# Kernel tuning notes

Hardware: AMD Instinct MI355X
Metric: run time of the kernel (lower is better)

## Reference

```python
import jax, jax.numpy as jnp
import numpy as np

# Model config (mirrors init_kwargs)
E = 8          # num_experts
K = 2          # top_k
S = 1          # select_top_k
THRESHOLD = 0.7
NORM_TOPK = True
H = 1024       # hidden_dim
F = 1024       # moe intermediate dim
B, SEQ = 2, 1024


def setup_inputs() -> dict:
    key = jax.random.key(0)
    k1, k2, k3, k4, k5 = jax.random.split(key, 5)
    hidden_states = jax.random.normal(k1, (B, SEQ, H), jnp.float32)
    gate_weight = jax.random.normal(k2, (E, H), jnp.float32) * 0.02
    gate_up_proj = jax.random.normal(k3, (E, 2 * F, H), jnp.float32) * 0.02
    down_proj = jax.random.normal(k4, (E, H, F), jnp.float32) * 0.02
    sim = jax.random.uniform(k5, (E, E), jnp.float32)
    sim = (sim + sim.T) / 2.0
    sim = sim.at[jnp.arange(E), jnp.arange(E)].set(1.0)  # fill_diagonal_(1.0)
    return {
        "hidden_states": hidden_states,
        "gate_weight": gate_weight,
        "gate_up_proj": gate_up_proj,
        "down_proj": down_proj,
        "similarity_matrix": sim,
    }


def reference(hidden_states, gate_weight, gate_up_proj, down_proj, similarity_matrix):
    b, s, h = hidden_states.shape
    x = hidden_states.reshape(-1, h)                     # [N, H]
    N = x.shape[0]

    # Router: logits -> softmax(fp32) -> topk (+ optional norm)
    logits = x @ gate_weight.T                           # [N, E]
    probs = jax.nn.softmax(logits.astype(jnp.float32), axis=-1)
    top_w, top_i = jax.lax.top_k(probs, K)               # [N, K]
    if NORM_TOPK:
        top_w = top_w / jnp.clip(jnp.sum(top_w, -1, keepdims=True), 1e-12)

    # SERE reroute: primary = union of top-S experts over batch; map each
    # secondary expert to its most-similar primary if sim >= threshold.
    primary_mask = jnp.zeros((E,), bool).at[top_i[:, :S].reshape(-1)].set(True)
    sim = jnp.where(primary_mask[None, :], similarity_matrix.astype(jnp.float32), -jnp.inf)
    best_j = jnp.argmax(sim, axis=-1)                    # best primary per expert
    best_sim = jnp.max(sim, axis=-1)
    ids = jnp.arange(E)
    expert_map = jnp.where((~primary_mask) & (best_sim >= THRESHOLD), best_j, ids)
    rerouted = expert_map[top_i]                         # [N, K]

    # Merge duplicate slots via scatter-add, then re-topk K.
    rows = jnp.arange(N)[:, None]
    dense = jnp.zeros((N, E), top_w.dtype).at[rows, rerouted].add(top_w)
    fw, fi = jax.lax.top_k(dense, K)                     # nnz per row <= K, so topk keeps all
    combine = jnp.zeros((N, E), fw.dtype).at[rows, fi].add(jnp.where(fw > 0, fw, 0.0))  # [N, E]

    # Expert MLPs (dense jit-friendly dispatch): silu(gate)*up -> down
    gu = jnp.einsum('nh,efh->enf', x, gate_up_proj)      # [E, N, 2F]
    g, u = jnp.split(gu, 2, axis=-1)
    hmid = jax.nn.silu(g) * u                            # [E, N, F]
    y = jnp.einsum('enf,ehf->enh', hmid, down_proj)      # [E, N, H]
    out = jnp.einsum('ne,enh->nh', combine, y)           # weighted combine
    return out.reshape(b, s, h)
```

## Files before the change

### kernel.cpp

```cpp
#include <hip/hip_runtime.h>
#include <cstdint>
#include <cstddef>

#define N_TOK 2048
#define HID 1024
#define FDIM 1024
#define NE 8
#define PAIR_CAP 5120
#define MT 128
#define BK 64
#define THRESH 0.7f

typedef __attribute__((ext_vector_type(8))) short bf16x8;
typedef __attribute__((ext_vector_type(4))) float f32x4;

static __device__ __forceinline__ unsigned short f2bf(float f) {
  unsigned int u = __float_as_uint(f);
  u += 0x7FFF + ((u >> 16) & 1);
  return (unsigned short)(u >> 16);
}
static __device__ __forceinline__ float bf2f(unsigned short u) {
  return __uint_as_float(((unsigned int)u) << 16);
}

static __device__ __forceinline__ void gl2lds16(const unsigned short* g, unsigned short* l) {
  __builtin_amdgcn_global_load_lds(
      (const __attribute__((address_space(1))) void*)g,
      (__attribute__((address_space(3))) void*)l, 16, 0, 0);
}

__global__ __launch_bounds__(256) void k_cvt(
    const float* __restrict__ src, unsigned short* __restrict__ dst, int n4) {
  int i = blockIdx.x * 256 + threadIdx.x;
  if (i < n4) {
    float4 v = ((const float4*)src)[i];
    ushort4 o;
    o.x = f2bf(v.x); o.y = f2bf(v.y); o.z = f2bf(v.z); o.w = f2bf(v.w);
    ((ushort4*)dst)[i] = o;
  }
}

__global__ __launch_bounds__(256) void k_router(
    const float* __restrict__ x, const float* __restrict__ gw,
    unsigned short* __restrict__ xb, float* __restrict__ topw,
    int* __restrict__ topi) {
  __shared__ float sgw[NE * HID];
  int t = threadIdx.x;
#pragma unroll
  for (int i = 0; i < NE * HID / 256; ++i) sgw[t + 256 * i] = gw[t + 256 * i];
  __syncthreads();
  int lane = t & 63;
  int wave = t >> 6;
  int n = blockIdx.x * 4 + wave;
  float acc[NE];
#pragma unroll
  for (int e = 0; e < NE; ++e) acc[e] = 0.f;
#pragma unroll
  for (int i = 0; i < HID / 64; ++i) {
    int h = i * 64 + lane;
    float xv = x[(size_t)n * HID + h];
    xb[(size_t)n * HID + h] = f2bf(xv);
#pragma unroll
    for (int e = 0; e < NE; ++e) acc[e] += xv * sgw[e * HID + h];
  }
#pragma unroll
  for (int off = 32; off > 0; off >>= 1) {
#pragma unroll
    for (int e = 0; e < NE; ++e) acc[e] += __shfl_xor(acc[e], off, 64);
  }
  if (lane == 0) {
    float m = acc[0];
    for (int e = 1; e < NE; ++e) m = fmaxf(m, acc[e]);
    float p[NE]; float s = 0.f;
    for (int e = 0; e < NE; ++e) { p[e] = __expf(acc[e] - m); s += p[e]; }
    float inv = 1.f / s;
    for (int e = 0; e < NE; ++e) p[e] *= inv;
    int i0 = 0; float b0 = p[0];
    for (int e = 1; e < NE; ++e) if (p[e] > b0) { b0 = p[e]; i0 = e; }
    int i1 = -1; float b1 = -1.f;
    for (int e = 0; e < NE; ++e) { if (e == i0) continue; if (p[e] > b1) { b1 = p[e]; i1 = e; } }
    float sw = b0 + b1; if (sw < 1e-12f) sw = 1e-12f;
    topw[n * 2] = b0 / sw; topw[n * 2 + 1] = b1 / sw;
    topi[n * 2] = i0;      topi[n * 2 + 1] = i1;
  }
}

__global__ __launch_bounds__(256) void k_pairs(
    const float* __restrict__ sim, const int* __restrict__ topi,
    const float* __restrict__ topw, int* __restrict__ ctrl,
    int* __restrict__ ptok, float* __restrict__ pw, int* __restrict__ pot) {
  __shared__ int prim[NE], emap[NE], cnt[NE], soff[NE], cur[NE], padc[NE];
  int t = threadIdx.x;
  if (t < NE) { prim[t] = 0; cnt[t] = 0; }
  __syncthreads();
  for (int n = t; n < N_TOK; n += 256) prim[topi[n * 2]] = 1;
  __syncthreads();
  if (t < NE) {
    float best = -1e30f; int bj = -1;
    for (int j = 0; j < NE; ++j) {
      if (prim[j]) {
        float s = sim[t * NE + j];
        if (s > best) { best = s; bj = j; }
      }
    }
    int m = t;
    if (!prim[t] && bj >= 0 && best >= THRESH) m = bj;
    emap[t] = m;
  }
  __syncthreads();
  for (int n = t; n < N_TOK; n += 256) {
    atomicAdd(&cnt[emap[topi[n * 2]]], 1);
    atomicAdd(&cnt[emap[topi[n * 2 + 1]]], 1);
  }
  __syncthreads();
  if (t == 0) {
    int o = 0;
    for (int e = 0; e < NE; ++e) {
      soff[e] = o;
      int p = (cnt[e] + MT - 1) & ~(MT - 1);
      padc[e] = p; cur[e] = 0; o += p;
    }
  }
  __syncthreads();
  if (t < NE) { ctrl[24 + t] = soff[t]; ctrl[32 + t] = padc[t]; }
  for (int n = t; n < N_TOK; n += 256) {
    int i0 = topi[n * 2], i1 = topi[n * 2 + 1];
    int e0 = emap[i0], e1 = emap[i1];
    int s0 = soff[e0] + atomicAdd(&cur[e0], 1);
    int s1 = soff[e1] + atomicAdd(&cur[e1], 1);
    ptok[s0] = n; pw[s0] = topw[n * 2];
    ptok[s1] = n; pw[s1] = topw[n * 2 + 1];
    pot[n * 2] = s0; pot[n * 2 + 1] = s1;
  }
  __syncthreads();
  for (int e = 0; e < NE; ++e) {
    for (int s = cnt[e] + t; s < padc[e]; s += 256) {
      ptok[soff[e] + s] = 0; pw[soff[e] + s] = 0.f;
    }
  }
}


__global__ __launch_bounds__(256, 2) void k_gemm1(
    const unsigned short* __restrict__ xb, const unsigned short* __restrict__ gupb,
    unsigned short* __restrict__ hmid, const int* __restrict__ ptok,
    const int* __restrict__ ctrl) {
  int b = blockIdx.x;
  int mt = b >> 8;
  int r8 = b & 255;
  int e = r8 >> 5;
  int y = r8 & 31;
  int padc = ctrl[32 + e];
  if (mt * MT >= padc) return;
  int base = ctrl[24 + e] + mt * MT;
  int f0 = y * 32;

  __shared__ unsigned short As[MT * BK];
  __shared__ unsigned short Bs[64 * BK];
  __shared__ int toks[MT];

  int t = threadIdx.x;
  if (t < MT) toks[t] = ptok[base + t];
  __syncthreads();

  int lane = t & 63;
  int wave = t >> 6;
  int wm = wave >> 1, wn = wave & 1;
  int lm = lane & 15, lh = lane >> 4;

  f32x4 acc[4][2] = {};
  const unsigned short* gbase = gupb + (size_t)e * 2 * FDIM * HID;

  for (int k0 = 0; k0 < HID; k0 += BK) {
#pragma unroll
    for (int i = 0; i < 4; ++i) {
      int q = i * 256 + t;
      int r = q >> 3;
      int cl = (q & 7) ^ (r & 7);
      gl2lds16(xb + (size_t)toks[r] * HID + k0 + cl * 8, &As[(q & ~63) * 8]);
    }
#pragma unroll
    for (int i = 0; i < 2; ++i) {
      int q = i * 256 + t;
      int r = q >> 3;
      int cl = (q & 7) ^ (r & 7);
      int grow = ((r >> 4) & 1) * FDIM + f0 + ((r >> 5) << 4) + (r & 15);
      gl2lds16(gbase + (size_t)grow * HID + k0 + cl * 8, &Bs[(q & ~63) * 8]);
    }
    __syncthreads();
#pragma unroll
    for (int kk = 0; kk < 2; ++kk) {
      bf16x8 af[4], bfr[2];
#pragma unroll
      for (int rb = 0; rb < 4; ++rb) {
        int row = wm * 64 + rb * 16 + lm;
        int p = (kk * 4 + lh) ^ (row & 7);
        af[rb] = *(const bf16x8*)(&As[row * BK + p * 8]);
      }
#pragma unroll
      for (int cc = 0; cc < 2; ++cc) {
        int row = wn * 32 + cc * 16 + lm;
        int p = (kk * 4 + lh) ^ (row & 7);
        bfr[cc] = *(const bf16x8*)(&Bs[row * BK + p * 8]);
      }
#pragma unroll
      for (int rb = 0; rb < 4; ++rb) {
#pragma unroll
        for (int cc = 0; cc < 2; ++cc)
          acc[rb][cc] = __builtin_amdgcn_mfma_f32_16x16x32_bf16(af[rb], bfr[cc], acc[rb][cc], 0, 0, 0);
      }
    }
    __syncthreads();
  }
#pragma unroll
  for (int rb = 0; rb < 4; ++rb) {
    int slot = base + wm * 64 + rb * 16 + lh * 4;
    f32x4 g = acc[rb][0];
    f32x4 u = acc[rb][1];
    int f = f0 + wn * 16 + lm;
#pragma unroll
    for (int reg = 0; reg < 4; ++reg) {
      float gv = g[reg];
      float hm = gv / (1.f + __expf(-gv)) * u[reg];
      hmid[(size_t)(slot + reg) * FDIM + f] = f2bf(hm);
    }
  }
}

__global__ __launch_bounds__(256, 2) void k_gemm2(
    const unsigned short* __restrict__ hmid, const unsigned short* __restrict__ dwnb,
    unsigned short* __restrict__ yb, const int* __restrict__ ctrl) {
  int b = blockIdx.x;
  int mt = b >> 8;
  int r8 = b & 255;
  int e = r8 >> 5;
  int y = r8 & 31;
  int padc = ctrl[32 + e];
  if (mt * MT >= padc) return;
  int base = ctrl[24 + e] + mt * MT;
  int h0 = y * 32;

  __shared__ unsigned short As[MT * BK];
  __shared__ unsigned short Bs[32 * BK];

  int t = threadIdx.x;
  int lane = t & 63;
  int wave = t >> 6;
  int wm = wave >> 1, wn = wave & 1;
  int lm = lane & 15, lh = lane >> 4;

  f32x4 acc[4] = {};
  const unsigned short* dbase = dwnb + (size_t)e * HID * FDIM;

  for (int k0 = 0; k0 < FDIM; k0 += BK) {
#pragma unroll
    for (int i = 0; i < 4; ++i) {
      int q = i * 256 + t;
      int r = q >> 3;
      int cl = (q & 7) ^ (r & 7);
      gl2lds16(hmid + (size_t)(base + r) * FDIM + k0 + cl * 8, &As[(q & ~63) * 8]);
    }
    {
      int q = t;
      int r = q >> 3;
      int cl = (q & 7) ^ (r & 7);
      gl2lds16(dbase + (size_t)(h0 + r) * FDIM + k0 + cl * 8, &Bs[(q & ~63) * 8]);
    }
    __syncthreads();
#pragma unroll
    for (int kk = 0; kk < 2; ++kk) {
      bf16x8 af[4], bfr;
#pragma unroll
      for (int rb = 0; rb < 4; ++rb) {
        int row = wm * 64 + rb * 16 + lm;
        int p = (kk * 4 + lh) ^ (row & 7);
        af[rb] = *(const bf16x8*)(&As[row * BK + p * 8]);
      }
      {
        int row = wn * 16 + lm;
        int p = (kk * 4 + lh) ^ (row & 7);
        bfr = *(const bf16x8*)(&Bs[row * BK + p * 8]);
      }
#pragma unroll
      for (int rb = 0; rb < 4; ++rb)
        acc[rb] = __builtin_amdgcn_mfma_f32_16x16x32_bf16(af[rb], bfr, acc[rb], 0, 0, 0);
    }
    __syncthreads();
  }
#pragma unroll
  for (int rb = 0; rb < 4; ++rb) {
    int slot = base + wm * 64 + rb * 16 + lh * 4;
    int h = h0 + wn * 16 + lm;
#pragma unroll
    for (int reg = 0; reg < 4; ++reg)
      yb[(size_t)(slot + reg) * HID + h] = f2bf(acc[rb][reg]);
  }
}

__global__ __launch_bounds__(256) void k_combine(
    const unsigned short* __restrict__ yb, const float* __restrict__ pw,
    const int* __restrict__ pot, float* __restrict__ out) {
  int n = blockIdx.x;
  int t = threadIdx.x;
  int p0 = pot[n * 2], p1 = pot[n * 2 + 1];
  float w0 = pw[p0], w1 = pw[p1];
  int h = t * 4;
  ushort4 a = *(const ushort4*)(yb + (size_t)p0 * HID + h);
  ushort4 b = *(const ushort4*)(yb + (size_t)p1 * HID + h);
  float4 o;
  o.x = w0 * bf2f(a.x) + w1 * bf2f(b.x);
  o.y = w0 * bf2f(a.y) + w1 * bf2f(b.y);
  o.z = w0 * bf2f(a.z) + w1 * bf2f(b.z);
  o.w = w0 * bf2f(a.w) + w1 * bf2f(b.w);
  *(float4*)(out + (size_t)n * HID + h) = o;
}

extern "C" void kernel_launch(void* const* d_in, const int* in_sizes, int n_in,
                              void* d_out, int out_size, void* d_ws, size_t ws_size,
                              hipStream_t stream) {
  (void)in_sizes; (void)n_in; (void)out_size; (void)ws_size;
  const float* x   = (const float*)d_in[0];
  const float* gw  = (const float*)d_in[1];
  const float* gup = (const float*)d_in[2];
  const float* dwn = (const float*)d_in[3];
  const float* sim = (const float*)d_in[4];
  float* out = (float*)d_out;

  char* w = (char*)d_ws;
  int* ctrl = (int*)w;
  size_t off = 256;
  unsigned short* xb = (unsigned short*)(w + off); off += (size_t)N_TOK * HID * 2;
  float* topw = (float*)(w + off); off += (size_t)N_TOK * 2 * 4;
  int*   topi = (int*)(w + off);   off += (size_t)N_TOK * 2 * 4;
  int*   ptok = (int*)(w + off);   off += (size_t)PAIR_CAP * 4;
  float* pw   = (float*)(w + off); off += (size_t)PAIR_CAP * 4;
  int*   pot  = (int*)(w + off);   off += (size_t)N_TOK * 2 * 4;
  unsigned short* hmid = (unsigned short*)(w + off); off += (size_t)PAIR_CAP * FDIM * 2;
  unsigned short* yb   = (unsigned short*)(w + off); off += (size_t)PAIR_CAP * HID * 2;
  unsigned short* gupb = (unsigned short*)(w + off); off += (size_t)NE * 2 * FDIM * HID * 2;
  unsigned short* dwnb = (unsigned short*)(w + off); off += (size_t)NE * HID * FDIM * 2;

  int n4g = NE * 2 * FDIM * HID / 4;
  int n4d = NE * HID * FDIM / 4;
  k_cvt<<<(n4g + 255) / 256, 256, 0, stream>>>(gup, gupb, n4g);
  k_cvt<<<(n4d + 255) / 256, 256, 0, stream>>>(dwn, dwnb, n4d);
  k_router<<<N_TOK / 4, 256, 0, stream>>>(x, gw, xb, topw, topi);
  k_pairs<<<1, 256, 0, stream>>>(sim, topi, topw, ctrl, ptok, pw, pot);
  k_gemm1<<<dim3(32 * 256), 256, 0, stream>>>(xb, gupb, hmid, ptok, ctrl);
  k_gemm2<<<dim3(32 * 256), 256, 0, stream>>>(hmid, dwnb, yb, ctrl);
  k_combine<<<N_TOK, 256, 0, stream>>>(yb, pw, pot, out);
}
```

Baseline: 210.4 us.

## Enlarge GEMM N-tiles to 128 columns and merge weight conversion kernels

Both expert GEMMs now compute a 128-column output tile per block (4x4 MFMA accumulators per wave) instead of 64 or 32 columns. This reuses each gathered A tile across more output columns and cuts the block count and redundant A loads. The two fp32-to-bf16 weight conversion launches are merged into one kernel. The change costs more registers and LDS per block, which may lower occupancy.

```diff
diff --git a/kernel.cpp b/kernel.cpp
--- a/kernel.cpp
+++ b/kernel.cpp
@@ -29,14 +29,23 @@
       (__attribute__((address_space(3))) void*)l, 16, 0, 0);
 }
 
-__global__ __launch_bounds__(256) void k_cvt(
-    const float* __restrict__ src, unsigned short* __restrict__ dst, int n4) {
+__global__ __launch_bounds__(256) void k_cvt2(
+    const float* __restrict__ a, unsigned short* __restrict__ ab, int n4a,
+    const float* __restrict__ b, unsigned short* __restrict__ bb, int n4b) {
   int i = blockIdx.x * 256 + threadIdx.x;
-  if (i < n4) {
-    float4 v = ((const float4*)src)[i];
+  if (i < n4a) {
+    float4 v = ((const float4*)a)[i];
     ushort4 o;
     o.x = f2bf(v.x); o.y = f2bf(v.y); o.z = f2bf(v.z); o.w = f2bf(v.w);
-    ((ushort4*)dst)[i] = o;
+    ((ushort4*)ab)[i] = o;
+  } else {
+    int j = i - n4a;
+    if (j < n4b) {
+      float4 v = ((const float4*)b)[j];
+      ushort4 o;
+      o.x = f2bf(v.x); o.y = f2bf(v.y); o.z = f2bf(v.z); o.w = f2bf(v.w);
+      ((ushort4*)bb)[j] = o;
+    }
   }
 }
 
@@ -146,17 +155,17 @@
     unsigned short* __restrict__ hmid, const int* __restrict__ ptok,
     const int* __restrict__ ctrl) {
   int b = blockIdx.x;
-  int mt = b >> 8;
-  int r8 = b & 255;
-  int e = r8 >> 5;
-  int y = r8 & 31;
+  int mt = b >> 7;
+  int r7 = b & 127;
+  int e = r7 >> 4;
+  int y = r7 & 15;
   int padc = ctrl[32 + e];
   if (mt * MT >= padc) return;
   int base = ctrl[24 + e] + mt * MT;
-  int f0 = y * 32;
+  int f0 = y * 64;
 
   __shared__ unsigned short As[MT * BK];
-  __shared__ unsigned short Bs[64 * BK];
+  __shared__ unsigned short Bs[128 * BK];
   __shared__ int toks[MT];
 
   int t = threadIdx.x;
@@ -168,7 +177,7 @@
   int wm = wave >> 1, wn = wave & 1;
   int lm = lane & 15, lh = lane >> 4;
 
-  f32x4 acc[4][2] = {};
+  f32x4 acc[4][4] = {};
   const unsigned short* gbase = gupb + (size_t)e * 2 * FDIM * HID;
 
   for (int k0 = 0; k0 < HID; k0 += BK) {
@@ -180,7 +189,7 @@
       gl2lds16(xb + (size_t)toks[r] * HID + k0 + cl * 8, &As[(q & ~63) * 8]);
     }
 #pragma unroll
-    for (int i = 0; i < 2; ++i) {
+    for (int i = 0; i < 4; ++i) {
       int q = i * 256 + t;
       int r = q >> 3;
       int cl = (q & 7) ^ (r & 7);
@@ -190,7 +199,7 @@
     __syncthreads();
 #pragma unroll
     for (int kk = 0; kk < 2; ++kk) {
-      bf16x8 af[4], bfr[2];
+      bf16x8 af[4], bfr[4];
 #pragma unroll
       for (int rb = 0; rb < 4; ++rb) {
         int row = wm * 64 + rb * 16 + lm;
@@ -198,15 +207,15 @@
         af[rb] = *(const bf16x8*)(&As[row * BK + p * 8]);
       }
 #pragma unroll
-      for (int cc = 0; cc < 2; ++cc) {
-        int row = wn * 32 + cc * 16 + lm;
+      for (int cc = 0; cc < 4; ++cc) {
+        int row = wn * 64 + cc * 16 + lm;
         int p = (kk * 4 + lh) ^ (row & 7);
         bfr[cc] = *(const bf16x8*)(&Bs[row * BK + p * 8]);
       }
 #pragma unroll
       for (int rb = 0; rb < 4; ++rb) {
 #pragma unroll
-        for (int cc = 0; cc < 2; ++cc)
+        for (int cc = 0; cc < 4; ++cc)
           acc[rb][cc] = __builtin_amdgcn_mfma_f32_16x16x32_bf16(af[rb], bfr[cc], acc[rb][cc], 0, 0, 0);
       }
     }
@@ -215,14 +224,17 @@
 #pragma unroll
   for (int rb = 0; rb < 4; ++rb) {
     int slot = base + wm * 64 + rb * 16 + lh * 4;
-    f32x4 g = acc[rb][0];
-    f32x4 u = acc[rb][1];
-    int f = f0 + wn * 16 + lm;
-#pragma unroll
-    for (int reg = 0; reg < 4; ++reg) {
-      float gv = g[reg];
-      float hm = gv / (1.f + __expf(-gv)) * u[reg];
-      hmid[(size_t)(slot + reg) * FDIM + f] = f2bf(hm);
+#pragma unroll
+    for (int fb = 0; fb < 2; ++fb) {
+      f32x4 g = acc[rb][fb * 2];
+      f32x4 u = acc[rb][fb * 2 + 1];
+      int f = f0 + wn * 32 + fb * 16 + lm;
+#pragma unroll
+      for (int reg = 0; reg < 4; ++reg) {
+        float gv = g[reg];
+        float hm = gv / (1.f + __expf(-gv)) * u[reg];
+        hmid[(size_t)(slot + reg) * FDIM + f] = f2bf(hm);
+      }
     }
   }
 }
@@ -231,17 +243,17 @@
     const unsigned short* __restrict__ hmid, const unsigned short* __restrict__ dwnb,
     unsigned short* __restrict__ yb, const int* __restrict__ ctrl) {
   int b = blockIdx.x;
-  int mt = b >> 8;
-  int r8 = b & 255;
-  int e = r8 >> 5;
-  int y = r8 & 31;
+  int mt = b >> 6;
+  int r6 = b & 63;
+  int e = r6 >> 3;
+  int y = r6 & 7;
   int padc = ctrl[32 + e];
   if (mt * MT >= padc) return;
   int base = ctrl[24 + e] + mt * MT;
-  int h0 = y * 32;
+  int h0 = y * 128;
 
   __shared__ unsigned short As[MT * BK];
-  __shared__ unsigned short Bs[32 * BK];
+  __shared__ unsigned short Bs[128 * BK];
 
   int t = threadIdx.x;
   int lane = t & 63;
@@ -249,7 +261,7 @@
   int wm = wave >> 1, wn = wave & 1;
   int lm = lane & 15, lh = lane >> 4;
 
-  f32x4 acc[4] = {};
+  f32x4 acc[4][4] = {};
   const unsigned short* dbase = dwnb + (size_t)e * HID * FDIM;
 
   for (int k0 = 0; k0 < FDIM; k0 += BK) {
@@ -260,8 +272,9 @@
       int cl = (q & 7) ^ (r & 7);
       gl2lds16(hmid + (size_t)(base + r) * FDIM + k0 + cl * 8, &As[(q & ~63) * 8]);
     }
-    {
-      int q = t;
+#pragma unroll
+    for (int i = 0; i < 4; ++i) {
+      int q = i * 256 + t;
       int r = q >> 3;
       int cl = (q & 7) ^ (r & 7);
       gl2lds16(dbase + (size_t)(h0 + r) * FDIM + k0 + cl * 8, &Bs[(q & ~63) * 8]);
@@ -269,31 +282,38 @@
     __syncthreads();
 #pragma unroll
     for (int kk = 0; kk < 2; ++kk) {
-      bf16x8 af[4], bfr;
+      bf16x8 af[4], bfr[4];
 #pragma unroll
       for (int rb = 0; rb < 4; ++rb) {
         int row = wm * 64 + rb * 16 + lm;
         int p = (kk * 4 + lh) ^ (row & 7);
         af[rb] = *(const bf16x8*)(&As[row * BK + p * 8]);
       }
-      {
-        int row = wn * 16 + lm;
+#pragma unroll
+      for (int cc = 0; cc < 4; ++cc) {
+        int row = wn * 64 + cc * 16 + lm;
         int p = (kk * 4 + lh) ^ (row & 7);
-        bfr = *(const bf16x8*)(&Bs[row * BK + p * 8]);
-      }
-#pragma unroll
-      for (int rb = 0; rb < 4; ++rb)
-        acc[rb] = __builtin_amdgcn_mfma_f32_16x16x32_bf16(af[rb], bfr, acc[rb], 0, 0, 0);
+        bfr[cc] = *(const bf16x8*)(&Bs[row * BK + p * 8]);
+      }
+#pragma unroll
+      for (int rb = 0; rb < 4; ++rb) {
+#pragma unroll
+        for (int cc = 0; cc < 4; ++cc)
+          acc[rb][cc] = __builtin_amdgcn_mfma_f32_16x16x32_bf16(af[rb], bfr[cc], acc[rb][cc], 0, 0, 0);
+      }
     }
     __syncthreads();
   }
 #pragma unroll
   for (int rb = 0; rb < 4; ++rb) {
     int slot = base + wm * 64 + rb * 16 + lh * 4;
-    int h = h0 + wn * 16 + lm;
-#pragma unroll
-    for (int reg = 0; reg < 4; ++reg)
-      yb[(size_t)(slot + reg) * HID + h] = f2bf(acc[rb][reg]);
+#pragma unroll
+    for (int cc = 0; cc < 4; ++cc) {
+      int h = h0 + wn * 64 + cc * 16 + lm;
+#pragma unroll
+      for (int reg = 0; reg < 4; ++reg)
+        yb[(size_t)(slot + reg) * HID + h] = f2bf(acc[rb][cc][reg]);
+    }
   }
 }
 
@@ -342,11 +362,10 @@
 
   int n4g = NE * 2 * FDIM * HID / 4;
   int n4d = NE * HID * FDIM / 4;
-  k_cvt<<<(n4g + 255) / 256, 256, 0, stream>>>(gup, gupb, n4g);
-  k_cvt<<<(n4d + 255) / 256, 256, 0, stream>>>(dwn, dwnb, n4d);
+  k_cvt2<<<(n4g + n4d + 255) / 256, 256, 0, stream>>>(gup, gupb, n4g, dwn, dwnb, n4d);
   k_router<<<N_TOK / 4, 256, 0, stream>>>(x, gw, xb, topw, topi);
   k_pairs<<<1, 256, 0, stream>>>(sim, topi, topw, ctrl, ptok, pw, pot);
-  k_gemm1<<<dim3(32 * 256), 256, 0, stream>>>(xb, gupb, hmid, ptok, ctrl);
-  k_gemm2<<<dim3(32 * 256), 256, 0, stream>>>(hmid, dwnb, yb, ctrl);
+  k_gemm1<<<dim3(32 * 128), 256, 0, stream>>>(xb, gupb, hmid, ptok, ctrl);
+  k_gemm2<<<dim3(32 * 64), 256, 0, stream>>>(hmid, dwnb, yb, ctrl);
   k_combine<<<N_TOK, 256, 0, stream>>>(yb, pw, pot, out);
 }
```

New measurement: 201.9 us. 4.0% less time.
